# Performance work log

Hardware: AMD Instinct MI355X
Metric: run time of the kernel (lower is better)

The kernel has to match this reference:

```python
import jax, jax.numpy as jnp
import numpy as np

SCORE_THRESH = 0.05
IOU_THRESH = 0.5
TOP_K = 1000      # candidates fed to NMS
MAX_DET = 100     # padded output detections


def _build_anchors(H, W):
    """Standard RetinaNet anchors: levels P3..P7, 3 ratios x 3 scales."""
    ratios = np.array([0.5, 1.0, 2.0])
    scales = np.array([2 ** 0, 2 ** (1.0 / 3.0), 2 ** (2.0 / 3.0)])
    all_anchors = []
    for lvl in [3, 4, 5, 6, 7]:
        stride = 2 ** lvl
        base_size = 2 ** (lvl + 2)
        # 9 base anchors centered at origin (ratio-major, scale-minor ordering)
        s = base_size * np.tile(scales, len(ratios))          # [9]
        r = np.repeat(ratios, len(scales))                    # [9]
        areas = s * s
        w = np.sqrt(areas / r)
        h = w * r
        base = np.stack([-w / 2, -h / 2, w / 2, h / 2], axis=1)  # [9,4]
        fh = (H + stride - 1) // stride
        fw = (W + stride - 1) // stride
        sx = (np.arange(fw) + 0.5) * stride
        sy = (np.arange(fh) + 0.5) * stride
        gx, gy = np.meshgrid(sx, sy)
        shifts = np.stack([gx.ravel(), gy.ravel(), gx.ravel(), gy.ravel()], axis=1)  # [fh*fw,4]
        all_anchors.append((shifts[:, None, :] + base[None, :, :]).reshape(-1, 4))
    return np.concatenate(all_anchors, axis=0).astype(np.float32)  # [A,4]


def setup_inputs() -> dict:
    key = jax.random.key(0)
    k1, k2 = jax.random.split(key)
    H = W = 1024
    C = 80
    anchors = jnp.asarray(_build_anchors(H, W))[None]            # [1,A,4]
    A = anchors.shape[1]
    classifications = jax.random.uniform(k1, (1, A, C), dtype=jnp.float32)
    regressions = jax.random.normal(k2, (1, A, 4), dtype=jnp.float32)
    return {"classifications": classifications, "regressions": regressions,
            "anchors": anchors, "img_h": H, "img_w": W}


def _decode_clip(anchors, regressions, img_h, img_w):
    # BBoxTransform with mean 0, std [0.1,0.1,0.2,0.2]
    aw = anchors[..., 2] - anchors[..., 0]
    ah = anchors[..., 3] - anchors[..., 1]
    acx = anchors[..., 0] + 0.5 * aw
    acy = anchors[..., 1] + 0.5 * ah
    dx = regressions[..., 0] * 0.1
    dy = regressions[..., 1] * 0.1
    dw = regressions[..., 2] * 0.2
    dh = regressions[..., 3] * 0.2
    pcx = acx + dx * aw
    pcy = acy + dy * ah
    pw = jnp.exp(dw) * aw
    ph = jnp.exp(dh) * ah
    boxes = jnp.stack([pcx - 0.5 * pw, pcy - 0.5 * ph,
                       pcx + 0.5 * pw, pcy + 0.5 * ph], axis=-1)
    # ClipBoxes
    lo = jnp.zeros(4, boxes.dtype)
    hi = jnp.array([img_w, img_h, img_w, img_h], boxes.dtype)
    return jnp.clip(boxes, lo, hi)  # [1,A,4]


def _nms_keep(boxes, valid):
    """Sequential greedy NMS over score-sorted boxes [K,4]; returns keep mask [K]."""
    K = boxes.shape[0]
    areas = jnp.maximum(boxes[:, 2] - boxes[:, 0], 0) * jnp.maximum(boxes[:, 3] - boxes[:, 1], 0)
    idx = jnp.arange(K)

    def body(i, keep):
        b = boxes[i]
        xx1 = jnp.maximum(b[0], boxes[:, 0])
        yy1 = jnp.maximum(b[1], boxes[:, 1])
        xx2 = jnp.minimum(b[2], boxes[:, 2])
        yy2 = jnp.minimum(b[3], boxes[:, 3])
        inter = jnp.maximum(xx2 - xx1, 0) * jnp.maximum(yy2 - yy1, 0)
        iou = inter / (areas[i] + areas - inter + 1e-8)
        suppress = (iou > IOU_THRESH) & (idx > i)
        return jnp.where(keep[i], keep & ~suppress, keep)

    return jax.lax.fori_loop(0, K, body, valid)


def reference(classifications, regressions, anchors, img_h, img_w):
    boxes = _decode_clip(anchors, regressions, img_h, img_w)       # [1,A,4]
    scores = jnp.max(classifications, axis=2)                      # [1,A]
    # Score threshold: mask out low scores, keep fixed shape (padded NMS)
    s0 = jnp.where(scores[0] > SCORE_THRESH, scores[0], -1.0)      # [A]
    top_scores, top_idx = jax.lax.top_k(s0, TOP_K)                 # sorted desc
    cand_boxes = boxes[0, top_idx]                                 # [K,4]
    keep = _nms_keep(cand_boxes, top_scores > SCORE_THRESH)        # [K]
    final = jnp.where(keep, top_scores, -1.0)
    det_scores, sel = jax.lax.top_k(final, MAX_DET)                # [100]
    det_idx = top_idx[sel]                                         # indices into A
    det_valid = det_scores > SCORE_THRESH
    cls = classifications[0, det_idx]                              # [100,C]
    nms_scores = jnp.where(det_valid, jnp.max(cls, axis=1), 0.0)
    nms_class = jnp.where(det_valid, jnp.argmax(cls, axis=1), -1)
    det_boxes = jnp.where(det_valid[:, None], boxes[0, det_idx], 0.0)
    return (nms_scores, nms_class, det_boxes)
```

## Files before the change

kernel.cpp:

```cpp
#include <hip/hip_runtime.h>
#include <stdint.h>

#define SCORE_THRESH 0.05f
#define IOU_THRESH 0.5f
#define TOP_K 1000
#define MAX_DET 100

#define UBINS 4096
#define NREP 4
#define CAND_CAP 2048
#define NMS_CHUNK 128

typedef unsigned int u32;
typedef unsigned long long u64;

#define OFF_HIST     0
#define OFF_STATE    65536
#define OFF_BAR      66560
#define MEMSET_LEN   82944
#define OFF_CAND     82944
#define OFF_RFLAG    99328
#define OFF_SIDX     103328
#define OFF_SSCORE   107328
#define OFF_CBOX     111328
#define OFF_M        127328
#define OFF_SCORES   255328

#define BAR_STRIDE_U32 1024

__device__ __forceinline__ u32 order_f32(float f) {
    u32 b = __float_as_uint(f);
    return (b & 0x80000000u) ? ~b : (b | 0x80000000u);
}

__device__ __forceinline__ u32 ubin(float s0) {
    float u = 1.0f - s0;
    u32 bin = __float_as_uint(u) >> 18;
    return bin > (UBINS - 1) ? (UBINS - 1) : bin;
}

__device__ __forceinline__ void st_sc(u32* p, u32 v)   { __hip_atomic_store(p, v, __ATOMIC_RELAXED, __HIP_MEMORY_SCOPE_AGENT); }
__device__ __forceinline__ void st_sc(float* p, float v){ __hip_atomic_store(p, v, __ATOMIC_RELAXED, __HIP_MEMORY_SCOPE_AGENT); }
__device__ __forceinline__ void st_sc(u64* p, u64 v)   { __hip_atomic_store(p, v, __ATOMIC_RELAXED, __HIP_MEMORY_SCOPE_AGENT); }
__device__ __forceinline__ u32  ld_sc(u32* p)          { return __hip_atomic_load(p, __ATOMIC_RELAXED, __HIP_MEMORY_SCOPE_AGENT); }

__device__ __forceinline__ void gbar(u32* barr, int k, int b, int G, bool dowait) {
    __syncthreads();
    u32* base = barr + (size_t)k * BAR_STRIDE_U32;
    if (threadIdx.x == 0) {
        asm volatile("s_waitcnt vmcnt(0)" ::: "memory");
        st_sc(&base[b], 1u);
    }
    if (!dowait) return;
    if (b == 0) {
        for (;;) {
            int my = 1;
            for (int i = (int)threadIdx.x; i < G; i += 256) my &= (int)ld_sc(&base[i]);
            if (__syncthreads_and(my)) break;
        }
        if (threadIdx.x == 0) st_sc(&base[512], 1u);
    } else {
        if (threadIdx.x == 0) {
            while (ld_sc(&base[512]) == 0u) __builtin_amdgcn_s_sleep(8);
        }
    }
    __syncthreads();
    asm volatile("" ::: "memory");
}

union ShMem {
    u32 hl[UBINS / 2];
    u32 wtot[4];
    struct { u32 wcnt[4]; u32 wbase[4]; u32 bbase; } cmp;
    struct { u64 ckeys[8]; u32 wpart[4][8]; } rank;
    struct {
        u64 Ml[2 * NMS_CHUNK * 16];
        u64 keepS[16];
        u32 nib[256];
        int act[TOP_K];
        u32 wsum[4];
        int nactS;
        int det[MAX_DET];
    } nms;
};

__global__ void __launch_bounds__(256, 2)
mega(const float* __restrict__ cls, const float* __restrict__ regs,
     const float* __restrict__ anchors, const int* __restrict__ pH,
     const int* __restrict__ pW, int A, int C,
     char* __restrict__ ws, float* __restrict__ out)
{
    __shared__ ShMem sh;
    __shared__ u32 shcut;
    u32*   hist   = (u32*)(ws + OFF_HIST);
    u32*   state  = (u32*)(ws + OFF_STATE);
    u32*   barr   = (u32*)(ws + OFF_BAR);
    u64*   cand   = (u64*)(ws + OFF_CAND);
    u32*   rflag  = (u32*)(ws + OFF_RFLAG);
    u32*   sidx   = (u32*)(ws + OFF_SIDX);
    float* sscore = (float*)(ws + OFF_SSCORE);
    float* cbox   = (float*)(ws + OFF_CBOX);
    u64*   M      = (u64*)(ws + OFF_M);
    float* scores = (float*)(ws + OFF_SCORES);

    const int t = threadIdx.x;
    const int b = blockIdx.x;
    const int G = gridDim.x;
    const int gid = b * 256 + t;
    const int gstride = G * 256;
    const int lane = t & 63, wv = t >> 6;

    if (C == 80) {
        for (int i = t; i < UBINS / 2; i += 256) sh.hl[i] = 0;
        __syncthreads();
        int sub = t & 3;
        int la  = t >> 2;
        int nstrips = (A + 63) >> 6;
        int per = (nstrips + G - 1) / G;
        for (int s = 0; s < per; s++) {
            int a = (b * per + s) * 64 + la;
            float m = -1e30f;
            if (a < A) {
                const float* p = cls + (size_t)a * 80 + sub * 4;
                #pragma unroll
                for (int k2 = 0; k2 < 5; k2++) {
                    float4 v = *(const float4*)(p + k2 * 16);
                    m = fmaxf(m, fmaxf(fmaxf(v.x, v.y), fmaxf(v.z, v.w)));
                }
            }
            m = fmaxf(m, __shfl_xor(m, 1, 64));
            m = fmaxf(m, __shfl_xor(m, 2, 64));
            if (sub == 0 && a < A) {
                float s0 = (m > SCORE_THRESH) ? m : -1.0f;
                st_sc(&scores[a], s0);
                u32 d = ubin(s0);
                atomicAdd(&sh.hl[d >> 1], (d & 1) ? 0x10000u : 1u);
            }
        }
        __syncthreads();
        u32* rep = hist + (size_t)(b & (NREP - 1)) * UBINS;
        for (int i = t; i < UBINS / 2; i += 256) {
            u32 v = sh.hl[i];
            if (v & 0xFFFFu) atomicAdd(&rep[2 * i],     v & 0xFFFFu);
            if (v >> 16)     atomicAdd(&rep[2 * i + 1], v >> 16);
        }
    } else {
        u32* rep = hist + (size_t)(b & (NREP - 1)) * UBINS;
        for (int a = gid; a < A; a += gstride) {
            const float* p = cls + (size_t)a * C;
            float m = -1e30f;
            for (int c = 0; c < C; c++) m = fmaxf(m, p[c]);
            float s0 = (m > SCORE_THRESH) ? m : -1.0f;
            st_sc(&scores[a], s0);
            atomicAdd(&rep[ubin(s0)], 1u);
        }
    }
    gbar(barr, 0, b, G, true);

    {
        if (t == 0) shcut = UBINS - 1;
        u32 cnt[16];
        #pragma unroll
        for (int i = 0; i < 16; i++) cnt[i] = 0;
        const uint4* hp = (const uint4*)hist;
        #pragma unroll
        for (int r = 0; r < NREP; r++) {
            #pragma unroll
            for (int i = 0; i < 4; i++) {
                uint4 v = hp[r * (UBINS / 4) + t * 4 + i];
                cnt[4*i]   += v.x; cnt[4*i+1] += v.y;
                cnt[4*i+2] += v.z; cnt[4*i+3] += v.w;
            }
        }
        u32 s = 0;
        #pragma unroll
        for (int i = 0; i < 16; i++) s += cnt[i];
        u32 x = s;
        for (int off = 1; off < 64; off <<= 1) {
            u32 v = (u32)__shfl_up((int)x, off, 64);
            if (lane >= off) x += v;
        }
        if (lane == 63) sh.wtot[wv] = x;
        __syncthreads();
        u32 below = x - s;
        for (int w = 0; w < wv; w++) below += sh.wtot[w];
        if (below < TOP_K && below + s >= TOP_K) {
            u32 cum = below;
            for (int i = 0; i < 16; i++) {
                cum += cnt[i];
                if (cum >= TOP_K) { shcut = (u32)(t * 16 + i); break; }
            }
        }
        __syncthreads();
    }
    const u32 cutbin = shcut;

    {
        int nr = (A + gstride - 1) / gstride;
        u32 mycnt = 0;
        for (int r = 0; r < nr; r++) {
            int a = gid + r * gstride;
            mycnt += ((a < A) && (ubin(scores[a]) <= cutbin)) ? 1u : 0u;
        }
        u32 wc = mycnt;
        wc += (u32)__shfl_xor((int)wc, 1, 64);
        wc += (u32)__shfl_xor((int)wc, 2, 64);
        wc += (u32)__shfl_xor((int)wc, 4, 64);
        wc += (u32)__shfl_xor((int)wc, 8, 64);
        wc += (u32)__shfl_xor((int)wc, 16, 64);
        wc += (u32)__shfl_xor((int)wc, 32, 64);
        if (lane == 0) sh.cmp.wcnt[wv] = wc;
        __syncthreads();
        if (t == 0) {
            u32 s = 0;
            #pragma unroll
            for (int w = 0; w < 4; w++) { sh.cmp.wbase[w] = s; s += sh.cmp.wcnt[w]; }
            sh.cmp.bbase = s ? atomicAdd(&state[5 * 32], s) : 0u;
        }
        __syncthreads();
        u32 off = sh.cmp.bbase + sh.cmp.wbase[wv];
        for (int r = 0; r < nr; r++) {
            int a = gid + r * gstride;
            float s0 = (a < A) ? scores[a] : 0.0f;
            bool pass = (a < A) && (ubin(s0) <= cutbin);
            u64 mask = __ballot(pass ? 1 : 0);
            if (pass) {
                u32 pos = off + (u32)__popcll(mask & ((1ull << lane) - 1ull));
                if (pos < CAND_CAP) {
                    u64 key = ((u64)order_f32(s0) << 32) | (u64)(0xFFFFFFFFu - (u32)a);
                    st_sc(&cand[pos], key);
                }
            }
            off += (u32)__popcll(mask);
        }
    }
    gbar(barr, 1, b, G, b < CAND_CAP / 8);

    if (b < CAND_CAP / 8) {
        int n = (int)state[5 * 32]; if (n > CAND_CAP) n = CAND_CAP;
        u64 kj[8];
        #pragma unroll
        for (int q = 0; q < 8; q++) {
            int j = t * 8 + q;
            kj[q] = (j < n) ? cand[j] : 0ull;
        }
        for (int bb = b; bb < CAND_CAP / 8; bb += G) {
            if (t < 8) {
                int c = bb * 8 + t;
                sh.rank.ckeys[t] = (c < n) ? cand[c] : 0ull;
            }
            __syncthreads();
            u64 ck[8];
            #pragma unroll
            for (int q = 0; q < 8; q++) ck[q] = sh.rank.ckeys[q];
            u32 cnt8[8] = {0,0,0,0,0,0,0,0};
            #pragma unroll
            for (int q = 0; q < 8; q++) {
                u64 kq = kj[q];
                #pragma unroll
                for (int q2 = 0; q2 < 8; q2++) cnt8[q2] += (kq > ck[q2]) ? 1u : 0u;
            }
            #pragma unroll
            for (int q2 = 0; q2 < 8; q2++) {
                u32 x = cnt8[q2];
                x += (u32)__shfl_xor((int)x, 1, 64);
                x += (u32)__shfl_xor((int)x, 2, 64);
                x += (u32)__shfl_xor((int)x, 4, 64);
                x += (u32)__shfl_xor((int)x, 8, 64);
                x += (u32)__shfl_xor((int)x, 16, 64);
                x += (u32)__shfl_xor((int)x, 32, 64);
                if (lane == 0) sh.rank.wpart[wv][q2] = x;
            }
            __syncthreads();
            if (t < 8) {
                int c = bb * 8 + t;
                if (c < n) {
                    u32 rank = sh.rank.wpart[0][t] + sh.rank.wpart[1][t]
                             + sh.rank.wpart[2][t] + sh.rank.wpart[3][t];
                    if (rank < TOP_K) {
                        u64 kk = ck[t];
                        u32 a = 0xFFFFFFFFu - (u32)(kk & 0xFFFFFFFFull);
                        u32 hi = (u32)(kk >> 32);
                        u32 bits = (hi & 0x80000000u) ? (hi & 0x7FFFFFFFu) : ~hi;
                        st_sc(&sidx[rank], a);
                        st_sc(&sscore[rank], __uint_as_float(bits));
                        float4 an = *(const float4*)(anchors + (size_t)a * 4);
                        float4 rg = *(const float4*)(regs + (size_t)a * 4);
                        float aw = an.z - an.x, ah = an.w - an.y;
                        float acx = an.x + 0.5f * aw, acy = an.y + 0.5f * ah;
                        float pcx = acx + (rg.x * 0.1f) * aw;
                        float pcy = acy + (rg.y * 0.1f) * ah;
                        float pw = expf(rg.z * 0.2f) * aw;
                        float ph = expf(rg.w * 0.2f) * ah;
                        float W = (float)(*pW), H = (float)(*pH);
                        st_sc(&cbox[rank * 4 + 0], fminf(fmaxf(pcx - 0.5f * pw, 0.0f), W));
                        st_sc(&cbox[rank * 4 + 1], fminf(fmaxf(pcy - 0.5f * ph, 0.0f), H));
                        st_sc(&cbox[rank * 4 + 2], fminf(fmaxf(pcx + 0.5f * pw, 0.0f), W));
                        st_sc(&cbox[rank * 4 + 3], fminf(fmaxf(pcy + 0.5f * ph, 0.0f), H));
                    }
                }
            }
            __syncthreads();
        }
    }
    gbar(barr, 2, b, G, b == 0 || (b - 1) * 4 < TOP_K);

    if (b >= 1) {
        const float4* B4 = (const float4*)cbox;
        for (int i = (b - 1) * 4 + wv; i < TOP_K; i += (G - 1) * 4) {
            float4 bi = B4[i];
            float ai = fmaxf(bi.z - bi.x, 0.0f) * fmaxf(bi.w - bi.y, 0.0f);
            u64 any = 0ull;
            int w0 = i >> 6;
            if (lane == 0)
                for (int w = 0; w < w0; w++) st_sc(&M[(size_t)i * 16 + w], 0ull);
            for (int w = w0; w < 16; w++) {
                int j = w * 64 + lane;
                bool sup = false;
                if (j < TOP_K && j > i) {
                    float4 bj = B4[j];
                    float aj = fmaxf(bj.z - bj.x, 0.0f) * fmaxf(bj.w - bj.y, 0.0f);
                    float xx1 = fmaxf(bi.x, bj.x), yy1 = fmaxf(bi.y, bj.y);
                    float xx2 = fminf(bi.z, bj.z), yy2 = fminf(bi.w, bj.w);
                    float inter = fmaxf(xx2 - xx1, 0.0f) * fmaxf(yy2 - yy1, 0.0f);
                    float iou = inter / (ai + aj - inter + 1e-8f);
                    sup = iou > IOU_THRESH;
                }
                u64 mask = __ballot(sup ? 1 : 0);
                if (lane == 0) { st_sc(&M[(size_t)i * 16 + w], mask); any |= mask; }
            }
            if (lane == 0) st_sc(&rflag[i], (any != 0ull) ? 1u : 0u);
        }
    } else {
        u32 nb = 0;
        int j0 = 4 * t;
        #pragma unroll
        for (int q = 0; q < 4; q++) {
            int j = j0 + q;
            if (j < TOP_K && sscore[j] > SCORE_THRESH) nb |= (1u << q);
        }
        sh.nms.nib[t] = nb;
        __syncthreads();
        if (t < 16) {
            u64 w = 0;
            for (int m2 = 0; m2 < 16; m2++)
                w |= ((u64)sh.nms.nib[t * 16 + m2]) << (4 * m2);
            sh.nms.keepS[t] = w;
        }
    }
    gbar(barr, 3, b, G, b == 0);

    if (b == 0) {
        u32 flags = 0; int cnt = 0;
        {
            int r0 = 4 * t;
            #pragma unroll
            for (int q = 0; q < 4; q++) {
                int r = r0 + q;
                if (r < TOP_K && rflag[r]) { flags |= (1u << q); cnt++; }
            }
        }
        int x = cnt;
        for (int off = 1; off < 64; off <<= 1) {
            int v = __shfl_up(x, off, 64);
            if (lane >= off) x += v;
        }
        if (lane == 63) sh.nms.wsum[wv] = (u32)x;
        __syncthreads();
        int base = 0;
        for (int w = 0; w < wv; w++) base += (int)sh.nms.wsum[w];
        int pos = base + x - cnt;
        {
            int r0 = 4 * t;
            #pragma unroll
            for (int q = 0; q < 4; q++)
                if (flags & (1u << q)) sh.nms.act[pos++] = r0 + q;
        }
        if (t == 0) {
            int na = 0;
            for (int w = 0; w < 4; w++) na += (int)sh.nms.wsum[w];
            sh.nms.nactS = na;
        }
        __syncthreads();
        int nact = sh.nms.nactS;
        int nchunks = (nact + NMS_CHUNK - 1) / NMS_CHUNK;

        if (nchunks > 0) {
            int cn0 = (nact < NMS_CHUNK) ? nact : NMS_CHUNK;
            for (int i = t; i < cn0 * 16; i += 256) {
                int row = sh.nms.act[i >> 4];
                sh.nms.Ml[i] = M[(size_t)row * 16 + (i & 15)];
            }
        }
        __syncthreads();
        u64 kp = (wv == 0 && lane < 16) ? sh.nms.keepS[lane] : 0ull;
        for (int ci = 0; ci < nchunks; ci++) {
            int c0 = ci * NMS_CHUNK;
            int cn = (nact - c0 < NMS_CHUNK) ? (nact - c0) : NMS_CHUNK;
            int cur = (ci & 1) * (NMS_CHUNK * 16);
            if (ci + 1 < nchunks && t >= 64) {
                int c0n = c0 + NMS_CHUNK;
                int cnn = (nact - c0n < NMS_CHUNK) ? (nact - c0n) : NMS_CHUNK;
                int nxt = ((ci + 1) & 1) * (NMS_CHUNK * 16);
                for (int i = t - 64; i < cnn * 16; i += 192) {
                    int row = sh.nms.act[c0n + (i >> 4)];
                    sh.nms.Ml[nxt + i] = M[(size_t)row * 16 + (i & 15)];
                }
            }
            if (wv == 0) {
                u64 mreg = (lane < 16 && cn > 0) ? sh.nms.Ml[cur + lane] : 0ull;
                for (int k = 0; k < cn; k++) {
                    u64 mnx = (lane < 16 && k + 1 < cn)
                            ? sh.nms.Ml[cur + (k + 1) * 16 + lane] : 0ull;
                    int i = sh.nms.act[c0 + k];
                    u64 kw = __shfl(kp, i >> 6, 64);
                    if ((kw >> (i & 63)) & 1ull) kp &= ~mreg;
                    mreg = mnx;
                }
            }
            __syncthreads();
        }
        if (wv == 0 && lane < 16) sh.nms.keepS[lane] = kp;
        __syncthreads();

        if (t == 0) {
            int cnt2 = 0;
            for (int w = 0; w < 16 && cnt2 < MAX_DET; w++) {
                u64 kw = sh.nms.keepS[w];
                while (kw && cnt2 < MAX_DET) {
                    int bbit = __ffsll((unsigned long long)kw) - 1;
                    sh.nms.det[cnt2++] = w * 64 + bbit;
                    kw &= kw - 1;
                }
            }
            for (; cnt2 < MAX_DET; cnt2++) sh.nms.det[cnt2] = -1;
        }
        __syncthreads();
        if (t < MAX_DET) {
            int i = sh.nms.det[t];
            if (i >= 0) {
                u32 a = sidx[i];
                const float* p = cls + (size_t)a * C;
                float best = -1e30f; int bc = 0;
                if (C == 80) {
                    #pragma unroll
                    for (int c4 = 0; c4 < 20; c4++) {
                        float4 v = *(const float4*)(p + c4 * 4);
                        if (v.x > best) { best = v.x; bc = c4 * 4; }
                        if (v.y > best) { best = v.y; bc = c4 * 4 + 1; }
                        if (v.z > best) { best = v.z; bc = c4 * 4 + 2; }
                        if (v.w > best) { best = v.w; bc = c4 * 4 + 3; }
                    }
                } else {
                    best = p[0]; bc = 0;
                    for (int c = 1; c < C; c++) {
                        float v = p[c];
                        if (v > best) { best = v; bc = c; }
                    }
                }
                out[t] = best;
                out[MAX_DET + t] = (float)bc;
                out[2 * MAX_DET + t * 4 + 0] = cbox[i * 4 + 0];
                out[2 * MAX_DET + t * 4 + 1] = cbox[i * 4 + 1];
                out[2 * MAX_DET + t * 4 + 2] = cbox[i * 4 + 2];
                out[2 * MAX_DET + t * 4 + 3] = cbox[i * 4 + 3];
            } else {
                out[t] = 0.0f;
                out[MAX_DET + t] = -1.0f;
                out[2 * MAX_DET + t * 4 + 0] = 0.0f;
                out[2 * MAX_DET + t * 4 + 1] = 0.0f;
                out[2 * MAX_DET + t * 4 + 2] = 0.0f;
                out[2 * MAX_DET + t * 4 + 3] = 0.0f;
            }
        }
    }
}

extern "C" void kernel_launch(void* const* d_in, const int* in_sizes, int n_in,
                              void* d_out, int out_size, void* d_ws, size_t ws_size,
                              hipStream_t stream) {
    (void)n_in; (void)out_size; (void)ws_size;
    const float* cls     = (const float*)d_in[0];
    const float* regs    = (const float*)d_in[1];
    const float* anchors = (const float*)d_in[2];
    const int*   pH      = (const int*)d_in[3];
    const int*   pW      = (const int*)d_in[4];
    int A = in_sizes[1] / 4;
    int C = in_sizes[0] / A;

    static int nCU = 0;
    if (nCU <= 0) {
        int dev = 0;
        hipGetDevice(&dev);
        hipDeviceGetAttribute(&nCU, hipDeviceAttributeMultiprocessorCount, dev);
        if (nCU <= 0) nCU = 256;
    }
    int G = 2 * nCU;
    if (G > 512) G = 512;
    if (G < 8) G = 8;

    char* ws = (char*)d_ws;
    hipMemsetAsync(ws, 0, MEMSET_LEN, stream);
    mega<<<dim3(G), dim3(256), 0, stream>>>(cls, regs, anchors, pH, pW, A, C,
                                            ws, (float*)d_out);
}
```

Baseline: 149.8 us.

## Scale grid to occupancy-limited size and retire extra blocks after histogram phase

Grid size now comes from the occupancy API (up to 4 blocks per CU, capped at 1024), and launch bounds are raised to allow 4 blocks per SM. This puts more blocks on the memory-bound class-max and histogram phase. After the first grid barrier, only the first 512 blocks continue. Later phases stride over that reduced count, and the barrier flag area is enlarged to match. The cost is higher register pressure from the tighter launch bounds and more blocks polling the first global barrier.

```diff
diff --git a/kernel.cpp b/kernel.cpp
--- a/kernel.cpp
+++ b/kernel.cpp
@@ -17,16 +17,16 @@
 #define OFF_HIST     0
 #define OFF_STATE    65536
 #define OFF_BAR      66560
-#define MEMSET_LEN   82944
-#define OFF_CAND     82944
-#define OFF_RFLAG    99328
-#define OFF_SIDX     103328
-#define OFF_SSCORE   107328
-#define OFF_CBOX     111328
-#define OFF_M        127328
-#define OFF_SCORES   255328
-
-#define BAR_STRIDE_U32 1024
+#define MEMSET_LEN   99328
+#define OFF_CAND     99328
+#define OFF_RFLAG    115712
+#define OFF_SIDX     119712
+#define OFF_SSCORE   123712
+#define OFF_CBOX     127712
+#define OFF_M        143712
+#define OFF_SCORES   271712
+
+#define BAR_STRIDE_U32 2048
 
 __device__ __forceinline__ u32 order_f32(float f) {
     u32 b = __float_as_uint(f);
@@ -44,7 +44,7 @@
 __device__ __forceinline__ void st_sc(u64* p, u64 v)   { __hip_atomic_store(p, v, __ATOMIC_RELAXED, __HIP_MEMORY_SCOPE_AGENT); }
 __device__ __forceinline__ u32  ld_sc(u32* p)          { return __hip_atomic_load(p, __ATOMIC_RELAXED, __HIP_MEMORY_SCOPE_AGENT); }
 
-__device__ __forceinline__ void gbar(u32* barr, int k, int b, int G, bool dowait) {
+__device__ __forceinline__ void gbar(u32* barr, int k, int b, int nflags, bool dowait) {
     __syncthreads();
     u32* base = barr + (size_t)k * BAR_STRIDE_U32;
     if (threadIdx.x == 0) {
@@ -55,13 +55,13 @@
     if (b == 0) {
         for (;;) {
             int my = 1;
-            for (int i = (int)threadIdx.x; i < G; i += 256) my &= (int)ld_sc(&base[i]);
+            for (int i = (int)threadIdx.x; i < nflags; i += 256) my &= (int)ld_sc(&base[i]);
             if (__syncthreads_and(my)) break;
         }
-        if (threadIdx.x == 0) st_sc(&base[512], 1u);
+        if (threadIdx.x == 0) st_sc(&base[1024], 1u);
     } else {
         if (threadIdx.x == 0) {
-            while (ld_sc(&base[512]) == 0u) __builtin_amdgcn_s_sleep(8);
+            while (ld_sc(&base[1024]) == 0u) __builtin_amdgcn_s_sleep(8);
         }
     }
     __syncthreads();
@@ -84,7 +84,7 @@
     } nms;
 };
 
-__global__ void __launch_bounds__(256, 2)
+__global__ void __launch_bounds__(256, 4)
 mega(const float* __restrict__ cls, const float* __restrict__ regs,
      const float* __restrict__ anchors, const int* __restrict__ pH,
      const int* __restrict__ pW, int A, int C,
@@ -106,6 +106,7 @@
     const int t = threadIdx.x;
     const int b = blockIdx.x;
     const int G = gridDim.x;
+    const int NP = (G < 512) ? G : 512;
     const int gid = b * 256 + t;
     const int gstride = G * 256;
     const int lane = t & 63, wv = t >> 6;
@@ -155,7 +156,14 @@
             atomicAdd(&rep[ubin(s0)], 1u);
         }
     }
-    gbar(barr, 0, b, G, true);
+    {
+        bool post = (b < NP);
+        gbar(barr, 0, b, G, post);
+        if (!post) return;
+    }
+
+    const int gid2 = b * 256 + t;
+    const int gstride2 = NP * 256;
 
     {
         if (t == 0) shcut = UBINS - 1;
@@ -196,10 +204,10 @@
     const u32 cutbin = shcut;
 
     {
-        int nr = (A + gstride - 1) / gstride;
+        int nr = (A + gstride2 - 1) / gstride2;
         u32 mycnt = 0;
         for (int r = 0; r < nr; r++) {
-            int a = gid + r * gstride;
+            int a = gid2 + r * gstride2;
             mycnt += ((a < A) && (ubin(scores[a]) <= cutbin)) ? 1u : 0u;
         }
         u32 wc = mycnt;
@@ -220,7 +228,7 @@
         __syncthreads();
         u32 off = sh.cmp.bbase + sh.cmp.wbase[wv];
         for (int r = 0; r < nr; r++) {
-            int a = gid + r * gstride;
+            int a = gid2 + r * gstride2;
             float s0 = (a < A) ? scores[a] : 0.0f;
             bool pass = (a < A) && (ubin(s0) <= cutbin);
             u64 mask = __ballot(pass ? 1 : 0);
@@ -234,7 +242,7 @@
             off += (u32)__popcll(mask);
         }
     }
-    gbar(barr, 1, b, G, b < CAND_CAP / 8);
+    gbar(barr, 1, b, NP, b < CAND_CAP / 8);
 
     if (b < CAND_CAP / 8) {
         int n = (int)state[5 * 32]; if (n > CAND_CAP) n = CAND_CAP;
@@ -244,7 +252,7 @@
             int j = t * 8 + q;
             kj[q] = (j < n) ? cand[j] : 0ull;
         }
-        for (int bb = b; bb < CAND_CAP / 8; bb += G) {
+        for (int bb = b; bb < CAND_CAP / 8; bb += NP) {
             if (t < 8) {
                 int c = bb * 8 + t;
                 sh.rank.ckeys[t] = (c < n) ? cand[c] : 0ull;
@@ -303,11 +311,11 @@
             __syncthreads();
         }
     }
-    gbar(barr, 2, b, G, b == 0 || (b - 1) * 4 < TOP_K);
+    gbar(barr, 2, b, NP, b == 0 || (b - 1) * 4 < TOP_K);
 
     if (b >= 1) {
         const float4* B4 = (const float4*)cbox;
-        for (int i = (b - 1) * 4 + wv; i < TOP_K; i += (G - 1) * 4) {
+        for (int i = (b - 1) * 4 + wv; i < TOP_K; i += (NP - 1) * 4) {
             float4 bi = B4[i];
             float ai = fmaxf(bi.z - bi.x, 0.0f) * fmaxf(bi.w - bi.y, 0.0f);
             u64 any = 0ull;
@@ -348,7 +356,7 @@
             sh.nms.keepS[t] = w;
         }
     }
-    gbar(barr, 3, b, G, b == 0);
+    gbar(barr, 3, b, NP, b == 0);
 
     if (b == 0) {
         u32 flags = 0; int cnt = 0;
@@ -488,16 +496,19 @@
     int A = in_sizes[1] / 4;
     int C = in_sizes[0] / A;
 
-    static int nCU = 0;
-    if (nCU <= 0) {
-        int dev = 0;
+    static int G = 0;
+    if (G <= 0) {
+        int dev = 0, nCU = 0, occ = 0;
         hipGetDevice(&dev);
         hipDeviceGetAttribute(&nCU, hipDeviceAttributeMultiprocessorCount, dev);
         if (nCU <= 0) nCU = 256;
-    }
-    int G = 2 * nCU;
-    if (G > 512) G = 512;
-    if (G < 8) G = 8;
+        hipOccupancyMaxActiveBlocksPerMultiprocessor(&occ, mega, 256, 0);
+        if (occ < 1) occ = 1;
+        if (occ > 4) occ = 4;
+        G = occ * nCU;
+        if (G > 1024) G = 1024;
+        if (G < 8) G = 8;
+    }
 
     char* ws = (char*)d_ws;
     hipMemsetAsync(ws, 0, MEMSET_LEN, stream);
```

Measured after the change: 153.5 us. 1.02x slower.
